# Kernel optimization log

Measured on AMD Instinct MI355X. Metric: run time of the kernel, lower is better.

Reference implementation:

```python
import jax, jax.numpy as jnp
import numpy as np
import math

B, T, D, H, L, V = 2, 1024, 768, 12, 4, 50257
HD = D // H
ROPE_PCT = 0.5
MAX_WL = 10000.0
EPS = 1e-5


def setup_inputs() -> dict:
    key = jax.random.key(0)
    ks = jax.random.split(key, 8)
    s = 0.02
    return {
        "idx": jax.random.randint(ks[0], (B, T), 0, V, dtype=jnp.int32),
        "wte": jax.random.normal(ks[1], (V, D), jnp.float32) * s,
        "ln1_g": jnp.ones((L, D), jnp.float32),
        "ln1_b": jnp.zeros((L, D), jnp.float32),
        "Wqkv": jax.random.normal(ks[2], (L, D, 3 * D), jnp.float32) * s,
        "bqkv": jnp.zeros((L, 3 * D), jnp.float32),
        "Wo": jax.random.normal(ks[3], (L, D, D), jnp.float32) * s,
        "bo": jnp.zeros((L, D), jnp.float32),
        "ln2_g": jnp.ones((L, D), jnp.float32),
        "ln2_b": jnp.zeros((L, D), jnp.float32),
        "Wfc": jax.random.normal(ks[4], (L, D, 4 * D), jnp.float32) * s,
        "bfc": jnp.zeros((L, 4 * D), jnp.float32),
        "Wp": jax.random.normal(ks[5], (L, 4 * D, D), jnp.float32) * s,
        "bp": jnp.zeros((L, D), jnp.float32),
        "lnf_g": jnp.ones((D,), jnp.float32),
        "lnf_b": jnp.zeros((D,), jnp.float32),
        "Wlm": jax.random.normal(ks[6], (D, V), jnp.float32) * s,
    }


def _ln(x, g, b):
    m = x.mean(-1, keepdims=True)
    v = x.var(-1, keepdims=True)
    return (x - m) / jnp.sqrt(v + EPS) * g + b


def _gelu(x):
    return 0.5 * x * (1.0 + jnp.tanh(math.sqrt(2.0 / math.pi) * (x + 0.044715 * x ** 3)))


def _p_rope(x, positions):
    # x: [B, H, T, HD]; partial RoPE: rotate first ROPE_PCT of angle pairs, leave rest.
    rope_angles = int(ROPE_PCT * HD // 2)
    nope_angles = HD // 2 - rope_angles
    fraction = 2.0 * jnp.arange(0, rope_angles) / HD
    timescale = jnp.power(MAX_WL, fraction)
    timescale = jnp.pad(timescale, (0, nope_angles), constant_values=jnp.inf)
    sinusoid = positions[:, None] / timescale[None, :]  # [T, HD//2]; pos/inf = 0 -> no rotation
    sin, cos = jnp.sin(sinusoid), jnp.cos(sinusoid)
    first, second = jnp.split(x, 2, axis=-1)
    out = jnp.concatenate([first * cos - second * sin, second * cos + first * sin], axis=-1)
    return out.astype(x.dtype)


def reference(idx, wte, ln1_g, ln1_b, Wqkv, bqkv, Wo, bo, ln2_g, ln2_b, Wfc, bfc, Wp, bp, lnf_g, lnf_b, Wlm):
    x = wte[idx]  # [B, T, D]
    positions = jnp.arange(T, dtype=x.dtype)
    causal = jnp.tril(jnp.ones((T, T), dtype=bool))
    scale = jnp.sqrt(jnp.float32(HD)).astype(x.dtype)
    for l in range(L):
        h1 = _ln(x, ln1_g[l], ln1_b[l])
        h2 = _ln(x, ln2_g[l], ln2_b[l])  # note: both LNs read the same x (as in source)
        # attention
        qkv = h1 @ Wqkv[l] + bqkv[l]
        q, k, v = jnp.split(qkv, 3, axis=-1)
        sh = lambda t: t.reshape(B, T, H, HD).transpose(0, 2, 1, 3)
        q, k, v = sh(q), sh(k), sh(v)
        q = _p_rope(q, positions)
        k = _p_rope(k, positions)
        att = jnp.einsum('bhqd,bhkd->bhqk', q, k) / scale
        att = jnp.where(causal, att, jnp.finfo(att.dtype).min)
        att = jax.nn.softmax(att, axis=-1)
        y = jnp.einsum('bhqk,bhkd->bhqd', att, v)
        y = y.transpose(0, 2, 1, 3).reshape(B, T, D)
        x = x + (y @ Wo[l] + bo[l])
        # MLP
        h = _gelu(h2 @ Wfc[l] + bfc[l])
        x = x + (h @ Wp[l] + bp[l])
    x = _ln(x, lnf_g, lnf_b)
    logits = x @ Wlm  # [B, T, V]
    return logits
```

## Files before the change

### kernel.cpp

```cpp
#include <hip/hip_runtime.h>

typedef unsigned short u16;
typedef unsigned int u32;
typedef __attribute__((ext_vector_type(8))) short bf16x8;
typedef __attribute__((ext_vector_type(4))) float f32x4;

#define SEQ 1024
#define DM 768
#define NH 12
#define HD2 64
#define NLAYER 4
#define NVOCAB 50257
#define BT 2048

__device__ __forceinline__ u16 f2bf(float f) {
  union { float f; u32 u; } v; v.f = f;
  u32 r = v.u + 0x7FFFu + ((v.u >> 16) & 1u);
  return (u16)(r >> 16);
}
__device__ __forceinline__ float bf2f(u16 u) {
  union { u32 u; float f; } v; v.u = ((u32)u) << 16;
  return v.f;
}

__device__ __forceinline__ void glds16(const u16* g, u16* l) {
  __builtin_amdgcn_global_load_lds(
      (const __attribute__((address_space(1))) u32*)(const void*)g,
      (__attribute__((address_space(3))) u32*)(void*)l, 16, 0, 0);
}

__global__ void k_embed(const int* __restrict__ idx, const float* __restrict__ wte,
                        float* __restrict__ xf) {
  int r = blockIdx.x;
  int tok = idx[r];
  const float* s = wte + (size_t)tok * DM;
  float* d = xf + (size_t)r * DM;
  for (int c = threadIdx.x; c < DM; c += 256) d[c] = s[c];
}

__global__ void k_trig(float* __restrict__ ctab, float* __restrict__ stab) {
  int gid = blockIdx.x * 256 + threadIdx.x;
  int tt = gid >> 4, j = gid & 15;
  float inv = powf(10000.f, -(float)j * (1.f / 32.f));
  float ang = (float)tt * inv;
  ctab[gid] = cosf(ang);
  stab[gid] = sinf(ang);
}

__global__ void k_cvtT(const float* __restrict__ in, u16* __restrict__ out,
                       int R, int C) {
  __shared__ u16 t[64][68];
  int c0 = blockIdx.x * 64, r0 = blockIdx.y * 64;
  int tx = threadIdx.x & 15, ty = threadIdx.x >> 4;
  int c = c0 + tx * 4;
#pragma unroll
  for (int i = 0; i < 4; ++i) {
    int r = r0 + ty + i * 16;
    float4 v = make_float4(0.f, 0.f, 0.f, 0.f);
    if (c + 3 < C) {
      v = *(const float4*)&in[(size_t)r * C + c];
    } else {
      if (c + 0 < C) v.x = in[(size_t)r * C + c];
      if (c + 1 < C) v.y = in[(size_t)r * C + c + 1];
      if (c + 2 < C) v.z = in[(size_t)r * C + c + 2];
      if (c + 3 < C) v.w = in[(size_t)r * C + c + 3];
    }
    t[ty + i * 16][tx * 4 + 0] = f2bf(v.x);
    t[ty + i * 16][tx * 4 + 1] = f2bf(v.y);
    t[ty + i * 16][tx * 4 + 2] = f2bf(v.z);
    t[ty + i * 16][tx * 4 + 3] = f2bf(v.w);
  }
  __syncthreads();
  int wl = threadIdx.x & 31, grp = threadIdx.x >> 5;
#pragma unroll
  for (int it = 0; it < 8; ++it) {
    int cc = it * 8 + grp;
    int gcol = c0 + cc;
    if (gcol < C) {
      u32 wv = (u32)t[2 * wl][cc] | ((u32)t[2 * wl + 1][cc] << 16);
      *(u32*)&out[(size_t)gcol * R + r0 + 2 * wl] = wv;
    }
  }
}

__device__ __forceinline__ float bsum(float v, float* red) {
#pragma unroll
  for (int o = 32; o > 0; o >>= 1) v += __shfl_down(v, o);
  if ((threadIdx.x & 63) == 0) red[threadIdx.x >> 6] = v;
  __syncthreads();
  if (threadIdx.x == 0) red[4] = red[0] + red[1] + red[2] + red[3];
  __syncthreads();
  return red[4];
}

__global__ void k_ln(const float* __restrict__ x, const float* __restrict__ g1,
                     const float* __restrict__ b1, const float* __restrict__ g2,
                     const float* __restrict__ b2, u16* __restrict__ o1,
                     u16* __restrict__ o2) {
  __shared__ float red[8];
  int r = blockIdx.x;
  int t = threadIdx.x;
  const float* xr = x + (size_t)r * DM;
  float v0 = xr[t], v1 = xr[t + 256], v2 = xr[t + 512];
  float mean = bsum(v0 + v1 + v2, red) * (1.f / DM);
  float d0 = v0 - mean, d1 = v1 - mean, d2 = v2 - mean;
  float var = bsum(d0 * d0 + d1 * d1 + d2 * d2, red) * (1.f / DM);
  float rstd = rsqrtf(var + 1e-5f);
  u16* p1 = o1 + (size_t)r * DM;
  p1[t]       = f2bf(d0 * rstd * g1[t]       + b1[t]);
  p1[t + 256] = f2bf(d1 * rstd * g1[t + 256] + b1[t + 256]);
  p1[t + 512] = f2bf(d2 * rstd * g1[t + 512] + b1[t + 512]);
  if (o2) {
    u16* p2 = o2 + (size_t)r * DM;
    p2[t]       = f2bf(d0 * rstd * g2[t]       + b2[t]);
    p2[t + 256] = f2bf(d1 * rstd * g2[t + 256] + b2[t + 256]);
    p2[t + 512] = f2bf(d2 * rstd * g2[t + 512] + b2[t + 512]);
  }
}

__global__ void k_attn(const u16* __restrict__ qr, const u16* __restrict__ kr,
                       const u16* __restrict__ vT, u16* __restrict__ yb) {
  int ti = (int)gridDim.x - 1 - (int)blockIdx.x;
  int bh = blockIdx.y;
  __shared__ u16 Ps[64 * 72];
  __shared__ u16 Ks[2][4096];
  __shared__ u16 Vs[2][4096];
  int tid = threadIdx.x;
  int rr = tid >> 2, cc = tid & 3;
  int w = tid >> 6, l = tid & 63;
  int rl = l & 15, g = l >> 4;
  {
    const u16* gq = qr + ((size_t)bh * SEQ + ti * 64 + rr) * HD2;
    *(uint4*)&Ps[rr * 72 + cc * 8]      = *(const uint4*)(gq + cc * 8);
    *(uint4*)&Ps[rr * 72 + cc * 8 + 32] = *(const uint4*)(gq + cc * 8 + 32);
  }
  int srow = w * 8 + (l >> 3);
  int gs = (l & 7) ^ (l >> 3);
  const u16* gkb = kr + (size_t)bh * SEQ * HD2;
  const u16* gvb = vT + (size_t)bh * HD2 * SEQ;
  glds16(gkb + (size_t)srow * 64 + gs * 8,        &Ks[0][w * 512]);
  glds16(gkb + (size_t)(32 + srow) * 64 + gs * 8, &Ks[0][2048 + w * 512]);
  glds16(gvb + (size_t)srow * SEQ + gs * 8,       &Vs[0][w * 512]);
  glds16(gvb + (size_t)(32 + srow) * SEQ + gs * 8,&Vs[0][2048 + w * 512]);
  __syncthreads();
  bf16x8 aq0 = *(const bf16x8*)&Ps[(w * 16 + rl) * 72 + g * 8];
  bf16x8 aq1 = *(const bf16x8*)&Ps[(w * 16 + rl) * 72 + 32 + g * 8];
  float m[4], lsum[4];
  f32x4 oacc[4] = {};
#pragma unroll
  for (int r2 = 0; r2 < 4; ++r2) { m[r2] = -3.0e38f; lsum[r2] = 0.f; }
  int qloc = w * 16 + g * 4;
  int sw = rl & 7;
  int cur = 0;
  for (int kt = 0; kt <= ti; ++kt) {
    if (kt < ti) {
      int nx = cur ^ 1;
      glds16(gkb + (size_t)((kt + 1) * 64 + srow) * 64 + gs * 8,      &Ks[nx][w * 512]);
      glds16(gkb + (size_t)((kt + 1) * 64 + 32 + srow) * 64 + gs * 8, &Ks[nx][2048 + w * 512]);
      glds16(gvb + (size_t)srow * SEQ + (kt + 1) * 64 + gs * 8,       &Vs[nx][w * 512]);
      glds16(gvb + (size_t)(32 + srow) * SEQ + (kt + 1) * 64 + gs * 8,&Vs[nx][2048 + w * 512]);
    }
    f32x4 s[4] = {};
    __builtin_amdgcn_s_setprio(1);
#pragma unroll
    for (int nt = 0; nt < 4; ++nt) {
      int r = (nt * 16 + rl) * 64;
      bf16x8 b0 = *(const bf16x8*)&Ks[cur][r + ((0 + g) ^ sw) * 8];
      bf16x8 b1 = *(const bf16x8*)&Ks[cur][r + ((4 + g) ^ sw) * 8];
      s[nt] = __builtin_amdgcn_mfma_f32_16x16x32_bf16(aq0, b0, s[nt], 0, 0, 0);
      s[nt] = __builtin_amdgcn_mfma_f32_16x16x32_bf16(aq1, b1, s[nt], 0, 0, 0);
    }
    __builtin_amdgcn_s_setprio(0);
#pragma unroll
    for (int nt = 0; nt < 4; ++nt) s[nt] *= 0.125f;
    if (kt == ti) {
#pragma unroll
      for (int nt = 0; nt < 4; ++nt) {
        int col = nt * 16 + rl;
#pragma unroll
        for (int r2 = 0; r2 < 4; ++r2)
          if (col > qloc + r2) s[nt][r2] = -3.0e38f;
      }
    }
#pragma unroll
    for (int r2 = 0; r2 < 4; ++r2) {
      float pm = fmaxf(fmaxf(s[0][r2], s[1][r2]), fmaxf(s[2][r2], s[3][r2]));
#pragma unroll
      for (int o = 1; o < 16; o <<= 1) pm = fmaxf(pm, __shfl_xor(pm, o));
      float mn = fmaxf(m[r2], pm);
      float corr = __expf(m[r2] - mn);
      float p0 = __expf(s[0][r2] - mn);
      float p1 = __expf(s[1][r2] - mn);
      float p2 = __expf(s[2][r2] - mn);
      float p3 = __expf(s[3][r2] - mn);
      float ps = p0 + p1 + p2 + p3;
#pragma unroll
      for (int o = 1; o < 16; o <<= 1) ps += __shfl_xor(ps, o);
      lsum[r2] = lsum[r2] * corr + ps;
      m[r2] = mn;
      oacc[0][r2] *= corr; oacc[1][r2] *= corr;
      oacc[2][r2] *= corr; oacc[3][r2] *= corr;
      int prow = (qloc + r2) * 72;
      Ps[prow + rl]      = f2bf(p0);
      Ps[prow + 16 + rl] = f2bf(p1);
      Ps[prow + 32 + rl] = f2bf(p2);
      Ps[prow + 48 + rl] = f2bf(p3);
    }
    bf16x8 pa0 = *(const bf16x8*)&Ps[(w * 16 + rl) * 72 + g * 8];
    bf16x8 pa1 = *(const bf16x8*)&Ps[(w * 16 + rl) * 72 + 32 + g * 8];
    __builtin_amdgcn_s_setprio(1);
#pragma unroll
    for (int nt = 0; nt < 4; ++nt) {
      int r = (nt * 16 + rl) * 64;
      bf16x8 b0 = *(const bf16x8*)&Vs[cur][r + ((0 + g) ^ sw) * 8];
      bf16x8 b1 = *(const bf16x8*)&Vs[cur][r + ((4 + g) ^ sw) * 8];
      oacc[nt] = __builtin_amdgcn_mfma_f32_16x16x32_bf16(pa0, b0, oacc[nt], 0, 0, 0);
      oacc[nt] = __builtin_amdgcn_mfma_f32_16x16x32_bf16(pa1, b1, oacc[nt], 0, 0, 0);
    }
    __builtin_amdgcn_s_setprio(0);
    __syncthreads();
    cur ^= 1;
  }
  int b = bh / NH, h = bh % NH;
  float invl[4];
#pragma unroll
  for (int r2 = 0; r2 < 4; ++r2) invl[r2] = 1.f / lsum[r2];
#pragma unroll
  for (int nt = 0; nt < 4; ++nt) {
    int d = nt * 16 + rl;
#pragma unroll
    for (int r2 = 0; r2 < 4; ++r2) {
      int trow = ti * 64 + qloc + r2;
      yb[((size_t)(b * SEQ + trow)) * DM + h * HD2 + d] = f2bf(oacc[nt][r2] * invl[r2]);
    }
  }
}

__global__ void k_logits(const u16* __restrict__ A, const u16* __restrict__ Bt,
                         float* __restrict__ outf, int M, int N, int K, int MT) {
  __shared__ u16 SM[16384];
  float* cw = (float*)SM;
  int nwg = gridDim.x;
  int id = blockIdx.x;
  if ((nwg & 7) == 0) id = (id & 7) * (nwg >> 3) + (id >> 3);
  int mt = id % MT, nt = id / MT;
  int m0 = mt * 128, n0 = nt * 128;
  int tid = threadIdx.x;
  int w = tid >> 6, l = tid & 63;
  int srow = w * 16 + (l >> 2);
  int gs = (l & 3) ^ ((l >> 3) & 3);
  const u16* gA0 = A + (size_t)(m0 + srow) * K + gs * 8;
  const u16* gA1 = A + (size_t)(m0 + 64 + srow) * K + gs * 8;
  int rb0 = n0 + srow;      if (rb0 > N - 1) rb0 = N - 1;
  int rb1 = n0 + 64 + srow; if (rb1 > N - 1) rb1 = N - 1;
  const u16* gB0 = Bt + (size_t)rb0 * K + gs * 8;
  const u16* gB1 = Bt + (size_t)rb1 * K + gs * 8;
  int wm = (w >> 1) * 64, wn = (w & 1) * 64;
  int rl = l & 15, g = l >> 4;
  int sla = g ^ ((rl >> 1) & 3);
  f32x4 acc[4][4] = {};
  int nK = K >> 5;
  int cur = 0;
  {
    u16* dA = SM + w * 512;
    glds16(gA0, dA); glds16(gA1, dA + 2048);
    u16* dB = SM + 4096 + w * 512;
    glds16(gB0, dB); glds16(gB1, dB + 2048);
  }
  __syncthreads();
  for (int kt = 0; kt < nK; ++kt) {
    if (kt + 1 < nK) {
      u16* dA = SM + (cur ^ 1) * 8192 + w * 512;
      glds16(gA0 + (kt + 1) * 32, dA); glds16(gA1 + (kt + 1) * 32, dA + 2048);
      u16* dB = dA + 4096;
      glds16(gB0 + (kt + 1) * 32, dB); glds16(gB1 + (kt + 1) * 32, dB + 2048);
    }
    const u16* As = SM + cur * 8192;
    const u16* Bs = As + 4096;
    bf16x8 af[4], bfr[4];
    __builtin_amdgcn_s_setprio(1);
#pragma unroll
    for (int i = 0; i < 4; ++i)
      af[i] = *(const bf16x8*)&As[(wm + i * 16 + rl) * 32 + sla * 8];
#pragma unroll
    for (int j = 0; j < 4; ++j)
      bfr[j] = *(const bf16x8*)&Bs[(wn + j * 16 + rl) * 32 + sla * 8];
#pragma unroll
    for (int i = 0; i < 4; ++i)
#pragma unroll
      for (int j = 0; j < 4; ++j)
        acc[i][j] = __builtin_amdgcn_mfma_f32_16x16x32_bf16(af[i], bfr[j],
                                                            acc[i][j], 0, 0, 0);
    __builtin_amdgcn_s_setprio(0);
    __syncthreads();
    cur ^= 1;
  }
  for (int ch = 0; ch < 4; ++ch) {
    if ((w >> 1) == (ch >> 1)) {
      int ib = (ch & 1) * 2;
#pragma unroll
      for (int ii = 0; ii < 2; ++ii) {
#pragma unroll
        for (int j = 0; j < 4; ++j) {
          int col = wn + j * 16 + rl;
#pragma unroll
          for (int r2 = 0; r2 < 4; ++r2) {
            int rowc = ii * 16 + g * 4 + r2;
            cw[rowc * 132 + col] = acc[ib + ii][j][r2];
          }
        }
      }
    }
    __syncthreads();
    for (int t = tid; t < 4096; t += 256) {
      int rowc = t >> 7, col = t & 127;
      int gc = n0 + col;
      if (gc < N)
        __builtin_nontemporal_store(cw[rowc * 132 + col],
                                    &outf[(size_t)(m0 + ch * 32 + rowc) * N + gc]);
    }
    __syncthreads();
  }
}

__global__ void k_gemm64(const u16* __restrict__ A, const u16* __restrict__ Bt,
                         const float* __restrict__ bias, u16* __restrict__ outb,
                         float* __restrict__ outf, int M, int N, int K, int MT,
                         int mode, const float* __restrict__ ctab,
                         const float* __restrict__ stab, u16* __restrict__ qrp,
                         u16* __restrict__ krp, u16* __restrict__ vTp) {
  __shared__ u16 SM2[16384];
  u16* As = SM2;
  u16* Bs = SM2 + 8192;
  float* cw = (float*)SM2;
  int nwg = gridDim.x;
  int id = blockIdx.x;
  if ((nwg & 7) == 0) id = (id & 7) * (nwg >> 3) + (id >> 3);
  int mt = id % MT, nt = id / MT;
  int sk = blockIdx.y, nsk = gridDim.y;
  int Kc = K / nsk, k0 = sk * Kc;
  int m0 = mt * 64, n0 = nt * 64;
  int tid = threadIdx.x;
  int w = tid >> 6, l = tid & 63;
  int row0 = tid >> 3, slot0 = tid & 7;
  int gs0 = slot0 ^ (row0 & 7);
  const u16* gA0 = A + (size_t)(m0 + row0) * K + k0 + gs0 * 8;
  const u16* gA1 = gA0 + (size_t)32 * K;
  const u16* gB0 = Bt + (size_t)(n0 + row0) * K + k0 + gs0 * 8;
  const u16* gB1 = gB0 + (size_t)32 * K;
  int wm = (w >> 1) * 32, wn = (w & 1) * 32;
  int rl = l & 15, g = l >> 4;
  int sl0 = g ^ (rl & 7), sl1 = (4 + g) ^ (rl & 7);
  f32x4 acc[2][2] = {};
  int nK = Kc >> 6;
  int cur = 0;
  {
    glds16(gA0, As + w * 512); glds16(gA1, As + 2048 + w * 512);
    glds16(gB0, Bs + w * 512); glds16(gB1, Bs + 2048 + w * 512);
  }
  __syncthreads();
  for (int kt = 0; kt < nK; ++kt) {
    if (kt + 1 < nK) {
      int nx = (cur ^ 1) * 4096;
      glds16(gA0 + (kt + 1) * 64, As + nx + w * 512);
      glds16(gA1 + (kt + 1) * 64, As + nx + 2048 + w * 512);
      glds16(gB0 + (kt + 1) * 64, Bs + nx + w * 512);
      glds16(gB1 + (kt + 1) * 64, Bs + nx + 2048 + w * 512);
    }
    const u16* Ac = As + cur * 4096;
    const u16* Bc = Bs + cur * 4096;
    bf16x8 a0[2], a1[2], b0[2], b1[2];
    __builtin_amdgcn_s_setprio(1);
#pragma unroll
    for (int i = 0; i < 2; ++i) {
      int r = (wm + i * 16 + rl) * 64;
      a0[i] = *(const bf16x8*)&Ac[r + sl0 * 8];
      a1[i] = *(const bf16x8*)&Ac[r + sl1 * 8];
    }
#pragma unroll
    for (int j = 0; j < 2; ++j) {
      int r = (wn + j * 16 + rl) * 64;
      b0[j] = *(const bf16x8*)&Bc[r + sl0 * 8];
      b1[j] = *(const bf16x8*)&Bc[r + sl1 * 8];
    }
#pragma unroll
    for (int i = 0; i < 2; ++i)
#pragma unroll
      for (int j = 0; j < 2; ++j) {
        acc[i][j] = __builtin_amdgcn_mfma_f32_16x16x32_bf16(a0[i], b0[j],
                                                            acc[i][j], 0, 0, 0);
        acc[i][j] = __builtin_amdgcn_mfma_f32_16x16x32_bf16(a1[i], b1[j],
                                                            acc[i][j], 0, 0, 0);
      }
    __builtin_amdgcn_s_setprio(0);
    __syncthreads();
    cur ^= 1;
  }
  if (mode != 4) {
#pragma unroll
    for (int i = 0; i < 2; ++i) {
#pragma unroll
      for (int j = 0; j < 2; ++j) {
        int col = n0 + wn + j * 16 + rl;
        float bv = bias ? bias[col] : 0.f;
#pragma unroll
        for (int r2 = 0; r2 < 4; ++r2) {
          int row = m0 + wm + i * 16 + g * 4 + r2;
          size_t oi = (size_t)row * N + col;
          float v = acc[i][j][r2];
          if (mode == 0) {
            outb[oi] = f2bf(v + bv);
          } else if (mode == 1) {
            v += bv;
            float u = 0.7978845608028654f * (v + 0.044715f * v * v * v);
            outb[oi] = f2bf(0.5f * v * (1.f + tanhf(u)));
          } else {
            if (sk == 0) v += bv;
            atomicAdd(&outf[oi], v);
          }
        }
      }
    }
    return;
  }
#pragma unroll
  for (int i = 0; i < 2; ++i) {
#pragma unroll
    for (int j = 0; j < 2; ++j) {
      int col = wn + j * 16 + rl;
      float bv = bias[n0 + col];
#pragma unroll
      for (int r2 = 0; r2 < 4; ++r2)
        cw[(wm + i * 16 + g * 4 + r2) * 68 + col] = acc[i][j][r2] + bv;
    }
  }
  __syncthreads();
  int reg = n0 / DM;
  int h = (n0 % DM) / 64;
  int b = m0 >> 10;
  int t0 = m0 & (SEQ - 1);
  size_t bh = (size_t)(b * NH + h);
  if (reg < 2) {
    u16* dst = (reg == 0) ? qrp : krp;
    for (int t = tid; t < 2048; t += 256) {
      int rowc = t >> 5, cp = t & 31;
      int d = 2 * cp;
      int tt = t0 + rowc;
      float x0 = cw[rowc * 68 + d];
      float x1 = cw[rowc * 68 + d + 1];
      float o0, o1;
      if (d < 32) {
        float y0 = cw[rowc * 68 + d + 32];
        float y1 = cw[rowc * 68 + d + 33];
        float c0 = 1.f, s0 = 0.f, c1 = 1.f, s1 = 0.f;
        if (d < 16) {
          c0 = ctab[tt * 16 + d];     s0 = stab[tt * 16 + d];
          c1 = ctab[tt * 16 + d + 1]; s1 = stab[tt * 16 + d + 1];
        }
        o0 = x0 * c0 - y0 * s0;
        o1 = x1 * c1 - y1 * s1;
      } else {
        int j = d - 32;
        float y0 = cw[rowc * 68 + j];
        float y1 = cw[rowc * 68 + j + 1];
        float c0 = 1.f, s0 = 0.f, c1 = 1.f, s1 = 0.f;
        if (j < 16) {
          c0 = ctab[tt * 16 + j];     s0 = stab[tt * 16 + j];
          c1 = ctab[tt * 16 + j + 1]; s1 = stab[tt * 16 + j + 1];
        }
        o0 = x0 * c0 + y0 * s0;
        o1 = x1 * c1 + y1 * s1;
      }
      u32 wv = (u32)f2bf(o0) | ((u32)f2bf(o1) << 16);
      *(u32*)&dst[(bh * SEQ + tt) * HD2 + d] = wv;
    }
  } else {
    for (int t = tid; t < 2048; t += 256) {
      int d = t >> 5, p = t & 31;
      int tt = t0 + 2 * p;
      u32 wv = (u32)f2bf(cw[(2 * p) * 68 + d]) |
               ((u32)f2bf(cw[(2 * p + 1) * 68 + d]) << 16);
      *(u32*)&vTp[(bh * HD2 + d) * SEQ + tt] = wv;
    }
  }
}

__global__ void k_gemm_f32b(const u16* __restrict__ A, const float* __restrict__ B,
                            float* __restrict__ outf, int M, int N, int K) {
  __shared__ u16 As[128 * 40];
  __shared__ u16 Bs[4 * 128 * 12];
  int tid = threadIdx.x;
  int wid = tid >> 6, lane = tid & 63;
  int rl = lane & 15, g = lane >> 4;
  int m0 = blockIdx.x * 128, n0 = blockIdx.y * 128;
  int wm = (wid >> 1) * 64, wn = (wid & 1) * 64;
  int ar = tid >> 2, ac = tid & 3;
  int bn = tid & 127, bq = tid >> 7;
  f32x4 acc[4][4] = {};
  int nK = K / 32;
  for (int kt = 0; kt < nK; ++kt) {
    __syncthreads();
    {
      const u16* ga = A + (size_t)(m0 + ar) * K + kt * 32 + ac * 8;
      *(uint4*)&As[ar * 40 + ac * 8] = *(const uint4*)ga;
      *(uint4*)&As[(ar + 64) * 40 + ac * 8] = *(const uint4*)(ga + (size_t)64 * K);
    }
    int col = n0 + bn;
#pragma unroll
    for (int r = 0; r < 4; ++r) {
      int kq = bq + 2 * r;
      int kk = kt * 32 + kq * 4;
      float f0 = 0.f, f1 = 0.f, f2v = 0.f, f3 = 0.f;
      if (col < N) {
        const float* gb = B + (size_t)kk * N + col;
        f0 = gb[0]; f1 = gb[(size_t)N]; f2v = gb[(size_t)2 * N]; f3 = gb[(size_t)3 * N];
      }
      uint2 wv;
      wv.x = (u32)f2bf(f0) | ((u32)f2bf(f1) << 16);
      wv.y = (u32)f2bf(f2v) | ((u32)f2bf(f3) << 16);
      *(uint2*)&Bs[(kq >> 1) * 1536 + bn * 12 + (kq & 1) * 4] = wv;
    }
    __syncthreads();
    bf16x8 af[4], bfr[4];
#pragma unroll
    for (int mt = 0; mt < 4; ++mt)
      af[mt] = *(const bf16x8*)&As[(wm + mt * 16 + rl) * 40 + g * 8];
#pragma unroll
    for (int nt = 0; nt < 4; ++nt) {
      const u16* p = &Bs[g * 1536 + (wn + nt * 16 + rl) * 12];
      union { bf16x8 v; uint2 u2[2]; } tmp;
      tmp.u2[0] = *(const uint2*)p;
      tmp.u2[1] = *(const uint2*)(p + 4);
      bfr[nt] = tmp.v;
    }
#pragma unroll
    for (int mt = 0; mt < 4; ++mt)
#pragma unroll
      for (int nt = 0; nt < 4; ++nt)
        acc[mt][nt] = __builtin_amdgcn_mfma_f32_16x16x32_bf16(af[mt], bfr[nt],
                                                              acc[mt][nt], 0, 0, 0);
  }
#pragma unroll
  for (int mt = 0; mt < 4; ++mt)
#pragma unroll
    for (int nt = 0; nt < 4; ++nt) {
      int col = n0 + wn + nt * 16 + rl;
      if (col >= N) continue;
#pragma unroll
      for (int r2 = 0; r2 < 4; ++r2) {
        int row = m0 + wm + mt * 16 + g * 4 + r2;
        outf[(size_t)row * N + col] = acc[mt][nt][r2];
      }
    }
}

extern "C" void kernel_launch(void* const* d_in, const int* in_sizes, int n_in,
                              void* d_out, int out_size, void* d_ws, size_t ws_size,
                              hipStream_t stream) {
  (void)in_sizes; (void)n_in; (void)out_size;
  const int*   idx  = (const int*)  d_in[0];
  const float* wte  = (const float*)d_in[1];
  const float* ln1g = (const float*)d_in[2];
  const float* ln1b = (const float*)d_in[3];
  const float* Wqkv = (const float*)d_in[4];
  const float* bqkv = (const float*)d_in[5];
  const float* Wo   = (const float*)d_in[6];
  const float* bo   = (const float*)d_in[7];
  const float* ln2g = (const float*)d_in[8];
  const float* ln2b = (const float*)d_in[9];
  const float* Wfc  = (const float*)d_in[10];
  const float* bfc  = (const float*)d_in[11];
  const float* Wp   = (const float*)d_in[12];
  const float* bp   = (const float*)d_in[13];
  const float* lnfg = (const float*)d_in[14];
  const float* lnfb = (const float*)d_in[15];
  const float* Wlm  = (const float*)d_in[16];
  float* out = (float*)d_out;

  char* sb = (char*)d_out;
  size_t off = 0;
  auto alloc = [&](size_t bytes) {
    char* p = sb + off;
    off += (bytes + 255) & ~(size_t)255;
    return (void*)p;
  };
  float* xf  = (float*)alloc((size_t)BT * DM * 4);
  u16* h1b   = (u16*)alloc((size_t)BT * DM * 2);
  u16* h2b   = (u16*)alloc((size_t)BT * DM * 2);
  u16* qr    = (u16*)alloc((size_t)BT * DM * 2);
  u16* kr    = (u16*)alloc((size_t)BT * DM * 2);
  u16* vT    = (u16*)alloc((size_t)BT * DM * 2);
  u16* yb    = (u16*)alloc((size_t)BT * DM * 2);
  u16* hgel  = (u16*)alloc((size_t)BT * 4 * DM * 2);
  float* ctab = (float*)alloc((size_t)SEQ * 16 * 4);
  float* stab = (float*)alloc((size_t)SEQ * 16 * 4);
  u16* wqkvT = (u16*)alloc((size_t)NLAYER * 3 * DM * DM * 2);
  u16* woT   = (u16*)alloc((size_t)NLAYER * DM * DM * 2);
  u16* wfcT  = (u16*)alloc((size_t)NLAYER * 4 * DM * DM * 2);
  u16* wpT   = (u16*)alloc((size_t)NLAYER * 4 * DM * DM * 2);

  size_t wlmT_bytes = (size_t)NVOCAB * DM * 2;
  size_t xlnf_bytes = (size_t)BT * DM * 2;
  bool fast_lm = ws_size >= wlmT_bytes + xlnf_bytes + 512;
  u16* wlmT = (u16*)d_ws;
  u16* xlnf = fast_lm ? (u16*)((char*)d_ws + ((wlmT_bytes + 255) & ~(size_t)255))
                      : (u16*)d_ws;

  k_trig<<<(SEQ * 16) / 256, 256, 0, stream>>>(ctab, stab);
  for (int l = 0; l < NLAYER; ++l) {
    k_cvtT<<<dim3((3 * DM + 63) / 64, DM / 64), 256, 0, stream>>>(
        Wqkv + (size_t)l * DM * 3 * DM, wqkvT + (size_t)l * 3 * DM * DM, DM, 3 * DM);
    k_cvtT<<<dim3(DM / 64, DM / 64), 256, 0, stream>>>(
        Wo + (size_t)l * DM * DM, woT + (size_t)l * DM * DM, DM, DM);
    k_cvtT<<<dim3((4 * DM) / 64, DM / 64), 256, 0, stream>>>(
        Wfc + (size_t)l * DM * 4 * DM, wfcT + (size_t)l * 4 * DM * DM, DM, 4 * DM);
    k_cvtT<<<dim3(DM / 64, (4 * DM) / 64), 256, 0, stream>>>(
        Wp + (size_t)l * 4 * DM * DM, wpT + (size_t)l * 4 * DM * DM, 4 * DM, DM);
  }
  if (fast_lm)
    k_cvtT<<<dim3((NVOCAB + 63) / 64, DM / 64), 256, 0, stream>>>(Wlm, wlmT, DM, NVOCAB);

  k_embed<<<BT, 256, 0, stream>>>(idx, wte, xf);
  for (int l = 0; l < NLAYER; ++l) {
    k_ln<<<BT, 256, 0, stream>>>(xf, ln1g + l * DM, ln1b + l * DM,
                                 ln2g + l * DM, ln2b + l * DM, h1b, h2b);
    k_gemm64<<<dim3((BT / 64) * (3 * DM / 64), 1), 256, 0, stream>>>(
        h1b, wqkvT + (size_t)l * 3 * DM * DM, bqkv + (size_t)l * 3 * DM,
        nullptr, nullptr, BT, 3 * DM, DM, BT / 64, 4, ctab, stab, qr, kr, vT);
    k_attn<<<dim3(SEQ / 64, 2 * NH), 256, 0, stream>>>(qr, kr, vT, yb);
    k_gemm64<<<dim3((BT / 64) * (DM / 64), 2), 256, 0, stream>>>(
        yb, woT + (size_t)l * DM * DM, bo + (size_t)l * DM,
        nullptr, xf, BT, DM, DM, BT / 64, 2, nullptr, nullptr, nullptr, nullptr, nullptr);
    k_gemm64<<<dim3((BT / 64) * (4 * DM / 64), 1), 256, 0, stream>>>(
        h2b, wfcT + (size_t)l * 4 * DM * DM, bfc + (size_t)l * 4 * DM,
        hgel, nullptr, BT, 4 * DM, DM, BT / 64, 1, nullptr, nullptr, nullptr, nullptr, nullptr);
    k_gemm64<<<dim3((BT / 64) * (DM / 64), 4), 256, 0, stream>>>(
        hgel, wpT + (size_t)l * 4 * DM * DM, bp + (size_t)l * DM,
        nullptr, xf, BT, DM, 4 * DM, BT / 64, 2, nullptr, nullptr, nullptr, nullptr, nullptr);
  }
  k_ln<<<BT, 256, 0, stream>>>(xf, lnfg, lnfb, nullptr, nullptr, xlnf, nullptr);
  if (fast_lm) {
    int nt = (NVOCAB + 127) / 128;
    k_logits<<<(BT / 128) * nt, 256, 0, stream>>>(
        xlnf, wlmT, out, BT, NVOCAB, DM, BT / 128);
  } else {
    k_gemm_f32b<<<dim3(BT / 128, (NVOCAB + 127) / 128), 256, 0, stream>>>(
        xlnf, Wlm, out, BT, NVOCAB, DM);
  }
}
```

Before: 978.3 us.

## Rewrite LM-head GEMM with 256x256 tiles, 8 waves and phased pipelining

```diff
diff --git a/kernel.cpp b/kernel.cpp
--- a/kernel.cpp
+++ b/kernel.cpp
@@ -236,90 +236,135 @@
   }
 }
 
-__global__ void k_logits(const u16* __restrict__ A, const u16* __restrict__ Bt,
-                         float* __restrict__ outf, int M, int N, int K, int MT) {
-  __shared__ u16 SM[16384];
-  float* cw = (float*)SM;
+#define LOADA8(BUFA, MH)                                                     \
+  {                                                                          \
+    _Pragma("unroll") for (int i_ = 0; i_ < 4; ++i_) {                       \
+      int row_ = wr * 128 + (MH) * 64 + i_ * 16 + rl;                        \
+      _Pragma("unroll") for (int ks_ = 0; ks_ < 2; ++ks_)                    \
+          af[i_][ks_] =                                                      \
+          *(const bf16x8*)&(BUFA)[row_ * 64 + (((ks_ << 2) + g) ^ sw7) * 8]; \
+    }                                                                        \
+  }
+#define LOADB8(BUFB, NHH, DST)                                               \
+  {                                                                          \
+    _Pragma("unroll") for (int jf_ = 0; jf_ < 2; ++jf_) {                    \
+      int row_ = wc * 64 + (NHH) * 32 + jf_ * 16 + rl;                       \
+      _Pragma("unroll") for (int ks_ = 0; ks_ < 2; ++ks_)                    \
+          DST[jf_][ks_] =                                                    \
+          *(const bf16x8*)&(BUFB)[row_ * 64 + (((ks_ << 2) + g) ^ sw7) * 8]; \
+    }                                                                        \
+  }
+#define STAGEA8(BUFA, T, H)                                                  \
+  if ((T) < nT) {                                                            \
+    _Pragma("unroll") for (int c_ = 0; c_ < 2; ++c_) {                       \
+      int rb_ = c_ * 128 + (H) * 64 + wid * 8;                               \
+      glds16(AL + (size_t)(m0 + rb_) * K + (size_t)(T) * 64,                 \
+             (BUFA) + rb_ * 64);                                             \
+    }                                                                        \
+  }
+#define STAGEB8(BUFB, T, H)                                                  \
+  if ((T) < nT) {                                                            \
+    _Pragma("unroll") for (int c_ = 0; c_ < 2; ++c_) {                       \
+      int rb_ = (2 * c_ + wr) * 64 + (H) * 32 + wc * 8;                      \
+      int sr_ = n0 + rb_ + lhi;                                              \
+      if (sr_ >= N) sr_ = N - 1;                                             \
+      glds16(Bt + (size_t)sr_ * K + (size_t)(T) * 64 + gsx * 8,              \
+             (BUFB) + rb_ * 64);                                             \
+    }                                                                        \
+  }
+#define PHSYNC8                                                              \
+  __builtin_amdgcn_sched_barrier(0);                                         \
+  __builtin_amdgcn_s_barrier();                                              \
+  asm volatile("s_waitcnt lgkmcnt(0)" ::: "memory");                         \
+  __builtin_amdgcn_sched_barrier(0);
+#define PHMFMA8(MH, NHH, BF)                                                 \
+  __builtin_amdgcn_s_setprio(1);                                             \
+  _Pragma("unroll") for (int i_ = 0; i_ < 4; ++i_)                           \
+  _Pragma("unroll") for (int jf_ = 0; jf_ < 2; ++jf_)                        \
+  _Pragma("unroll") for (int ks_ = 0; ks_ < 2; ++ks_)                        \
+      acc[(MH)*4 + i_][(NHH)*2 + jf_] =                                      \
+      __builtin_amdgcn_mfma_f32_16x16x32_bf16(                               \
+          af[i_][ks_], BF[jf_][ks_], acc[(MH)*4 + i_][(NHH)*2 + jf_],        \
+          0, 0, 0);                                                          \
+  __builtin_amdgcn_s_setprio(0);                                             \
+  __builtin_amdgcn_s_barrier();
+
+__global__ __launch_bounds__(512, 2) void k_logits8(
+    const u16* __restrict__ A, const u16* __restrict__ Bt,
+    float* __restrict__ outf, int M, int N, int K, int MT) {
+  __shared__ u16 SM[65536];
+  (void)M;
   int nwg = gridDim.x;
   int id = blockIdx.x;
   if ((nwg & 7) == 0) id = (id & 7) * (nwg >> 3) + (id >> 3);
   int mt = id % MT, nt = id / MT;
-  int m0 = mt * 128, n0 = nt * 128;
+  int m0 = mt * 256, n0 = nt * 256;
   int tid = threadIdx.x;
-  int w = tid >> 6, l = tid & 63;
-  int srow = w * 16 + (l >> 2);
-  int gs = (l & 3) ^ ((l >> 3) & 3);
-  const u16* gA0 = A + (size_t)(m0 + srow) * K + gs * 8;
-  const u16* gA1 = A + (size_t)(m0 + 64 + srow) * K + gs * 8;
-  int rb0 = n0 + srow;      if (rb0 > N - 1) rb0 = N - 1;
-  int rb1 = n0 + 64 + srow; if (rb1 > N - 1) rb1 = N - 1;
-  const u16* gB0 = Bt + (size_t)rb0 * K + gs * 8;
-  const u16* gB1 = Bt + (size_t)rb1 * K + gs * 8;
-  int wm = (w >> 1) * 64, wn = (w & 1) * 64;
-  int rl = l & 15, g = l >> 4;
-  int sla = g ^ ((rl >> 1) & 3);
-  f32x4 acc[4][4] = {};
-  int nK = K >> 5;
-  int cur = 0;
-  {
-    u16* dA = SM + w * 512;
-    glds16(gA0, dA); glds16(gA1, dA + 2048);
-    u16* dB = SM + 4096 + w * 512;
-    glds16(gB0, dB); glds16(gB1, dB + 2048);
-  }
-  __syncthreads();
-  for (int kt = 0; kt < nK; ++kt) {
-    if (kt + 1 < nK) {
-      u16* dA = SM + (cur ^ 1) * 8192 + w * 512;
-      glds16(gA0 + (kt + 1) * 32, dA); glds16(gA1 + (kt + 1) * 32, dA + 2048);
-      u16* dB = dA + 4096;
-      glds16(gB0 + (kt + 1) * 32, dB); glds16(gB1 + (kt + 1) * 32, dB + 2048);
-    }
-    const u16* As = SM + cur * 8192;
-    const u16* Bs = As + 4096;
-    bf16x8 af[4], bfr[4];
-    __builtin_amdgcn_s_setprio(1);
-#pragma unroll
-    for (int i = 0; i < 4; ++i)
-      af[i] = *(const bf16x8*)&As[(wm + i * 16 + rl) * 32 + sla * 8];
-#pragma unroll
-    for (int j = 0; j < 4; ++j)
-      bfr[j] = *(const bf16x8*)&Bs[(wn + j * 16 + rl) * 32 + sla * 8];
-#pragma unroll
-    for (int i = 0; i < 4; ++i)
-#pragma unroll
-      for (int j = 0; j < 4; ++j)
-        acc[i][j] = __builtin_amdgcn_mfma_f32_16x16x32_bf16(af[i], bfr[j],
-                                                            acc[i][j], 0, 0, 0);
-    __builtin_amdgcn_s_setprio(0);
+  int wid = tid >> 6, l = tid & 63;
+  int wr = wid >> 2, wc = wid & 3;
+  int rl = l & 15, g = l >> 4, sw7 = rl & 7;
+  int lhi = l >> 3;
+  int gsx = (l & 7) ^ lhi;
+  const u16* AL = A + (size_t)lhi * K + gsx * 8;
+  int nT = K >> 6;
+  int nIter = nT >> 1;
+  u16* pA0 = SM;
+  u16* pB0 = SM + 16384;
+  u16* pA1 = SM + 32768;
+  u16* pB1 = SM + 49152;
+  f32x4 acc[8][4] = {};
+  bf16x8 af[4][2], bf0[2][2], bf1[2][2];
+  STAGEA8(pA0, 0, 0) STAGEB8(pB0, 0, 0) STAGEA8(pA0, 0, 1) STAGEB8(pB0, 0, 1)
+  STAGEA8(pA1, 1, 0) STAGEB8(pB1, 1, 0)
+  asm volatile("s_waitcnt vmcnt(4)" ::: "memory");
+  __builtin_amdgcn_s_barrier();
+  for (int it = 0; it < nIter; ++it) {
+    int ta = 2 * it, tb = ta + 1;
+    bool lastIt = (it + 1 == nIter);
+    LOADA8(pA0, 0) LOADB8(pB0, 0, bf0) STAGEA8(pA1, tb, 1)
+    PHSYNC8 PHMFMA8(0, 0, bf0)
+    LOADB8(pB0, 1, bf1) STAGEB8(pB1, tb, 1)
+    PHSYNC8 PHMFMA8(0, 1, bf1)
+    LOADA8(pA0, 1) STAGEA8(pA0, ta + 2, 0)
+    PHSYNC8 PHMFMA8(1, 0, bf0)
+    STAGEB8(pB0, ta + 2, 0)
+    if (!lastIt) asm volatile("s_waitcnt vmcnt(4)" ::: "memory");
+    else         asm volatile("s_waitcnt vmcnt(0)" ::: "memory");
+    PHSYNC8 PHMFMA8(1, 1, bf1)
+    LOADA8(pA1, 0) LOADB8(pB1, 0, bf0) STAGEA8(pA0, ta + 2, 1)
+    PHSYNC8 PHMFMA8(0, 0, bf0)
+    LOADB8(pB1, 1, bf1) STAGEB8(pB0, ta + 2, 1)
+    PHSYNC8 PHMFMA8(0, 1, bf1)
+    LOADA8(pA1, 1) STAGEA8(pA1, tb + 2, 0)
+    PHSYNC8 PHMFMA8(1, 0, bf0)
+    STAGEB8(pB1, tb + 2, 0)
+    if (!lastIt) asm volatile("s_waitcnt vmcnt(4)" ::: "memory");
+    PHSYNC8 PHMFMA8(1, 1, bf1)
+  }
+  float* cw = (float*)SM;
+  for (int ch = 0; ch < 8; ++ch) {
     __syncthreads();
-    cur ^= 1;
-  }
-  for (int ch = 0; ch < 4; ++ch) {
-    if ((w >> 1) == (ch >> 1)) {
-      int ib = (ch & 1) * 2;
+    if (wr == (ch >> 2)) {
 #pragma unroll
       for (int ii = 0; ii < 2; ++ii) {
-#pragma unroll
-        for (int j = 0; j < 4; ++j) {
-          int col = wn + j * 16 + rl;
-#pragma unroll
-          for (int r2 = 0; r2 < 4; ++r2) {
-            int rowc = ii * 16 + g * 4 + r2;
-            cw[rowc * 132 + col] = acc[ib + ii][j][r2];
-          }
+        int ig = (ch & 3) * 2 + ii;
+#pragma unroll
+        for (int jg = 0; jg < 4; ++jg) {
+          int col = wc * 64 + jg * 16 + rl;
+#pragma unroll
+          for (int r2 = 0; r2 < 4; ++r2)
+            cw[(ii * 16 + g * 4 + r2) * 260 + col] = acc[ig][jg][r2];
         }
       }
     }
     __syncthreads();
-    for (int t = tid; t < 4096; t += 256) {
-      int rowc = t >> 7, col = t & 127;
+    for (int t = tid; t < 8192; t += 512) {
+      int rw = t >> 8, col = t & 255;
       int gc = n0 + col;
       if (gc < N)
-        __builtin_nontemporal_store(cw[rowc * 132 + col],
-                                    &outf[(size_t)(m0 + ch * 32 + rowc) * N + gc]);
-    }
-    __syncthreads();
+        __builtin_nontemporal_store(
+            cw[rw * 260 + col], &outf[(size_t)(m0 + ch * 32 + rw) * N + gc]);
+    }
   }
 }
 
@@ -640,9 +685,9 @@
   }
   k_ln<<<BT, 256, 0, stream>>>(xf, lnfg, lnfb, nullptr, nullptr, xlnf, nullptr);
   if (fast_lm) {
-    int nt = (NVOCAB + 127) / 128;
-    k_logits<<<(BT / 128) * nt, 256, 0, stream>>>(
-        xlnf, wlmT, out, BT, NVOCAB, DM, BT / 128);
+    int nt = (NVOCAB + 255) / 256;
+    k_logits8<<<(BT / 256) * nt, 512, 0, stream>>>(
+        xlnf, wlmT, out, BT, NVOCAB, DM, BT / 256);
   } else {
     k_gemm_f32b<<<dim3(BT / 128, (NVOCAB + 127) / 128), 256, 0, stream>>>(
         xlnf, Wlm, out, BT, NVOCAB, DM);
```

Measured after the change: 1.020 ms. 4.3% more time.
